# Optimization experiments

Measured on AMD Instinct MI355X. Metric: run time of the kernel, lower is better.

## Reference

```python
import jax, jax.numpy as jnp
import numpy as np

P2 = 8
BN_EPS = 1e-5


def _slice_maps(p2):
    # Faithfully reproduce the buggy fs[:, i*j-1] indexing: later loop
    # iterations overwrite earlier ones; slots never written stay zero.
    last = {}
    for i in range(1, p2 + 1):
        for j in range(1, p2 + 1):
            last[i * j - 1] = (i - 1, j - 1)
    src_i = np.zeros(p2 * p2, np.int32)
    src_j = np.zeros(p2 * p2, np.int32)
    mask = np.zeros(p2 * p2, np.float32)
    for k, (ii, jj) in last.items():
        src_i[k], src_j[k], mask[k] = ii, jj, 1.0
    # unslice: output patch (i,j) reads slot (i+1)*(j+1)-1
    uns = np.array([[(i + 1) * (j + 1) - 1 for j in range(p2)] for i in range(p2)], np.int32)
    return src_i, src_j, mask, uns


def setup_inputs() -> dict:
    key = jax.random.key(0)
    ks = jax.random.split(key, 16)
    C, N, p2 = 32, 8, P2
    s = 0.05
    inp = {
        "x": jax.random.normal(ks[0], (8, C, 512, 512), jnp.float32),
        "w30": jax.random.normal(ks[1], (N, C, 3, 3), jnp.float32) * s,
        "b30": jnp.zeros((N,), jnp.float32),
        "w10": jax.random.normal(ks[2], (C, C), jnp.float32) * s,
        "b10": jnp.zeros((C,), jnp.float32),
        "w11": jax.random.normal(ks[3], (N, N), jnp.float32) * s,
        "b11": jnp.zeros((N,), jnp.float32),
        "w12a": jax.random.normal(ks[4], (p2, p2 * p2), jnp.float32) * s,
        "b12a": jnp.zeros((p2,), jnp.float32),
        "w12b": jax.random.normal(ks[5], (p2, p2), jnp.float32) * s,
        "b12b": jnp.zeros((p2,), jnp.float32),
        "w12c": jax.random.normal(ks[6], (p2 * p2, p2), jnp.float32) * s,
        "b12c": jnp.zeros((p2 * p2,), jnp.float32),
        "w31": jax.random.normal(ks[7], (C, C), jnp.float32) * s,
        "b31": jnp.zeros((C,), jnp.float32),
        "bn_gamma": jnp.ones((C,), jnp.float32),
        "bn_beta": jnp.zeros((C,), jnp.float32),
        "bn_mean": jnp.zeros((C,), jnp.float32),
        "bn_var": jnp.ones((C,), jnp.float32),
    }
    return inp


def reference(x, w30, b30, w10, b10, w11, b11, w12a, b12a, w12b, b12b,
              w12c, b12c, w31, b31, bn_gamma, bn_beta, bn_mean, bn_var):
    p2 = P2
    b, C, H, W = x.shape
    h, wd = H // p2, W // p2
    L = h * wd
    N = w30.shape[0]
    src_i, src_j, mask_np, uns = _slice_maps(p2)

    # --- slice into patches (with the original's overwrite/zero semantics) ---
    patches = x.reshape(b, C, p2, h, p2, wd).transpose(0, 2, 4, 1, 3, 5)  # [b,p2,p2,C,h,w]
    fs = patches[:, src_i, src_j] * jnp.asarray(mask_np)[None, :, None, None, None]
    fs = fs.reshape(b * p2 * p2, C, h, wd)

    # --- graph_convolution ---
    B = jax.lax.conv_general_dilated(fs, w30, (1, 1), 'SAME',
            dimension_numbers=('NCHW', 'OIHW', 'NCHW')) + b30[None, :, None, None]
    B = jax.nn.relu(B)                                    # [bp, N, h, w]
    B1 = B.reshape(b * p2 * p2, N, L)
    fs1 = fs.reshape(b * p2 * p2, C, L)
    fs2 = jnp.einsum('bnl,bcl->bnc', B1, fs1)              # [bp, N, C]
    fs3 = jax.nn.relu(jnp.einsum('on,bnc->boc', w11, fs2) + b11[None, :, None])
    fs5 = jax.nn.relu(jnp.einsum('oc,bcn->bon', w10, fs3.transpose(0, 2, 1)) + b10[None, :, None])  # [bp,C,N]
    fs6 = jnp.einsum('bnl,bcn->bcl', B1, fs5)              # [bp, C, L]
    fs6 = fs6.reshape(b, p2 * p2, C, h, wd)

    fg = x.reshape(b, C, 8, H // 8, 8, W // 8).mean(axis=(3, 5))  # [b,C,8,8]
    fg1 = fg.reshape(b, C, p2 * p2).transpose(0, 2, 1)            # [b, p2^2, C]
    g = jax.nn.relu(jnp.einsum('ok,bkc->boc', w12a, fg1) + b12a[None, :, None])
    g = jax.nn.relu(jnp.einsum('ok,bkc->boc', w12b, g) + b12b[None, :, None])
    g = jax.nn.sigmoid(jnp.einsum('ok,bkc->boc', w12c, g) + b12c[None, :, None])  # [b,p2^2,C]
    out5 = g[:, :, :, None, None] * fs6                            # [b,p2^2,C,h,w]

    # --- unslice back to image (patch (i,j) reads slot (i+1)*(j+1)-1) ---
    gathered = out5[:, uns]                                        # [b,p2,p2,C,h,w]
    out = gathered.transpose(0, 3, 1, 4, 2, 5).reshape(b, C, H, W)

    # --- conv31: 1x1 conv + BatchNorm(eval) + ReLU, residual add ---
    y = jnp.einsum('oc,bchw->bohw', w31, out) + b31[None, :, None, None]
    y = (y - bn_mean[None, :, None, None]) * jax.lax.rsqrt(bn_var[None, :, None, None] + BN_EPS)
    y = jax.nn.relu(y * bn_gamma[None, :, None, None] + bn_beta[None, :, None, None])
    return y + x
```

## Files before the change

### kernel.cpp

```cpp
#include <hip/hip_runtime.h>
#include <math.h>
#include <stdint.h>

#define HW 512
#define NACT 30
#define NINACT 34

struct Maps {
    int src_i[64];
    int src_j[64];
    int mask[64];
    int aidx[64];
    int act_k[NACT];
    int inact_k[NINACT];
};

static Maps make_maps() {
    Maps m;
    for (int k = 0; k < 64; k++) { m.src_i[k]=0; m.src_j[k]=0; m.mask[k]=0; m.aidx[k]=-1; }
    for (int i = 1; i <= 8; i++)
        for (int j = 1; j <= 8; j++) {
            int k = i*j-1;
            m.src_i[k]=i-1; m.src_j[k]=j-1; m.mask[k]=1;
        }
    int cnt=0, icnt=0;
    for (int k=0;k<64;k++) {
        if (m.mask[k]) { m.aidx[k]=cnt; if (cnt < NACT) m.act_k[cnt]=k; cnt++; }
        else           { if (icnt < NINACT) m.inact_k[icnt]=k; icnt++; }
    }
    return m;
}

__global__ __launch_bounds__(256) void k_zero(float* __restrict__ p, int n) {
    int i = blockIdx.x*256 + threadIdx.x;
    if (i < n) p[i] = 0.f;
}

__global__ __launch_bounds__(256) void k_fg(const float* __restrict__ x, float* __restrict__ fgw, Maps m) {
    int blk = blockIdx.x;
    int q = blk % NINACT;
    int bc = blk / NINACT;
    int c = bc & 31;
    int b = bc >> 5;
    int k = m.inact_k[q];
    int pi = k >> 3, pj = k & 7;
    const float* xp = x + (size_t)(b*32+c)*HW*HW;
    int t = threadIdx.x;
    float s = 0.f;
    #pragma unroll
    for (int ii = 0; ii < 4; ii++) {
        int idx4 = t + 256*ii;
        int y = idx4 >> 4;
        int xx = (idx4 & 15) * 4;
        float4 v = *(const float4*)(xp + (size_t)(pi*64 + y)*HW + pj*64 + xx);
        s += v.x + v.y + v.z + v.w;
    }
    for (int off = 32; off > 0; off >>= 1) s += __shfl_down(s, off);
    __shared__ float p[4];
    if ((t & 63) == 0) p[t >> 6] = s;
    __syncthreads();
    if (t == 0) {
        float tot = p[0]+p[1]+p[2]+p[3];
        fgw[(b*64 + k)*32 + c] = tot * (1.0f/4096.0f);
    }
}

__global__ void k_g(const float* __restrict__ fgw,
                    const float* __restrict__ w12a, const float* __restrict__ b12a,
                    const float* __restrict__ w12b, const float* __restrict__ b12b,
                    const float* __restrict__ w12c, const float* __restrict__ b12c,
                    float* __restrict__ g) {
    int b = blockIdx.x;
    int c = threadIdx.x;
    if (c >= 32) return;
    float fg[64];
    #pragma unroll
    for (int k = 0; k < 64; k++) fg[k] = fgw[(b*64+k)*32 + c];
    float g1[8], g2[8];
    #pragma unroll
    for (int o = 0; o < 8; o++) {
        float v = b12a[o];
        #pragma unroll
        for (int k2 = 0; k2 < 64; k2++) v += w12a[o*64+k2]*fg[k2];
        g1[o] = fmaxf(v, 0.f);
    }
    #pragma unroll
    for (int o = 0; o < 8; o++) {
        float v = b12b[o];
        #pragma unroll
        for (int k2 = 0; k2 < 8; k2++) v += w12b[o*8+k2]*g1[k2];
        g2[o] = fmaxf(v, 0.f);
    }
    for (int o = 0; o < 64; o++) {
        float v = b12c[o];
        #pragma unroll
        for (int k2 = 0; k2 < 8; k2++) v += w12c[o*8+k2]*g2[k2];
        g[(b*64+o)*32 + c] = 1.f / (1.f + expf(-v));
    }
}

__global__ __launch_bounds__(256, 8) void k_conv(
        const float* __restrict__ x, const float* __restrict__ w30,
        const float* __restrict__ b30, float* __restrict__ B, Maps m) {
    int blk = blockIdx.x;
    int rt = blockIdx.y;
    int a = blk % NACT, b = blk / NACT;
    int k = m.act_k[a];
    int spi = m.src_i[k], spj = m.src_j[k];
    int r0 = rt*8;

    __shared__ float wlc[288];
    __shared__ __align__(16) float xs[4*10*72];

    int t = threadIdx.x;
    for (int idx = t; idx < 4*10*72; idx += 256) xs[idx] = 0.f;

    int col = t & 63, tl = t >> 6;
    float acc[2][8];
    #pragma unroll
    for (int rr=0; rr<2; rr++)
        #pragma unroll
        for (int n=0;n<8;n++) acc[rr][n]=0.f;

    const float* xb = x + (size_t)b*32*HW*HW;

    for (int c0 = 0; c0 < 32; c0 += 4) {
        __syncthreads();
        for (int idx = t; idx < 288; idx += 256) {
            int cc = idx / 72;
            int rem = idx - cc*72;
            wlc[idx] = w30[((rem & 7)*32 + c0 + cc)*9 + (rem >> 3)];
        }
        for (int idx = t; idx < 640; idx += 256) {
            int cc = idx / 160;
            int rem = idx - cc*160;
            int r = rem >> 4;
            int q = rem & 15;
            int pr = r0 - 1 + r;
            float4 v = make_float4(0.f,0.f,0.f,0.f);
            if (pr >= 0 && pr < 64)
                v = *(const float4*)(xb + (size_t)(c0+cc)*HW*HW + (size_t)(spi*64+pr)*HW + spj*64 + q*4);
            *(float4*)(xs + cc*720 + r*72 + 4 + q*4) = v;
        }
        __syncthreads();
        #pragma unroll
        for (int cc = 0; cc < 4; cc++) {
            const float* xrow = xs + cc*720 + (tl*2)*72 + 3 + col;
            const float* wb = wlc + cc*72;
            #pragma unroll
            for (int dy = 0; dy < 3; dy++) {
                float xa0 = xrow[dy*72 + 0];
                float xa1 = xrow[dy*72 + 1];
                float xa2 = xrow[dy*72 + 2];
                float xb0 = xrow[dy*72 + 72];
                float xb1 = xrow[dy*72 + 73];
                float xb2 = xrow[dy*72 + 74];
                #pragma unroll
                for (int dx = 0; dx < 3; dx++) {
                    float4 wa0 = *(const float4*)(wb + (dy*3+dx)*8);
                    float4 wa1 = *(const float4*)(wb + (dy*3+dx)*8 + 4);
                    float x0 = (dx==0) ? xa0 : ((dx==1) ? xa1 : xa2);
                    float x1 = (dx==0) ? xb0 : ((dx==1) ? xb1 : xb2);
                    acc[0][0] = fmaf(x0, wa0.x, acc[0][0]);
                    acc[0][1] = fmaf(x0, wa0.y, acc[0][1]);
                    acc[0][2] = fmaf(x0, wa0.z, acc[0][2]);
                    acc[0][3] = fmaf(x0, wa0.w, acc[0][3]);
                    acc[0][4] = fmaf(x0, wa1.x, acc[0][4]);
                    acc[0][5] = fmaf(x0, wa1.y, acc[0][5]);
                    acc[0][6] = fmaf(x0, wa1.z, acc[0][6]);
                    acc[0][7] = fmaf(x0, wa1.w, acc[0][7]);
                    acc[1][0] = fmaf(x1, wa0.x, acc[1][0]);
                    acc[1][1] = fmaf(x1, wa0.y, acc[1][1]);
                    acc[1][2] = fmaf(x1, wa0.z, acc[1][2]);
                    acc[1][3] = fmaf(x1, wa0.w, acc[1][3]);
                    acc[1][4] = fmaf(x1, wa1.x, acc[1][4]);
                    acc[1][5] = fmaf(x1, wa1.y, acc[1][5]);
                    acc[1][6] = fmaf(x1, wa1.z, acc[1][6]);
                    acc[1][7] = fmaf(x1, wa1.w, acc[1][7]);
                }
            }
        }
    }
    float* Bp = B + (size_t)(b*NACT+a)*8*4096;
    #pragma unroll
    for (int rr=0; rr<2; rr++) {
        int y = r0 + tl*2 + rr;
        #pragma unroll
        for (int n=0;n<8;n++)
            Bp[n*4096 + y*64 + col] = fmaxf(acc[rr][n] + b30[n], 0.f);
    }
}

__global__ __launch_bounds__(256, 8) void k_fs2a(
        const float* __restrict__ x, const float* __restrict__ B,
        float* __restrict__ fs2g, float* __restrict__ fgw, Maps m) {
    int blk = blockIdx.x;
    int rt = blockIdx.y;
    int a = blk % NACT, b = blk / NACT;
    int k = m.act_k[a];
    int spi = m.src_i[k], spj = m.src_j[k];
    int l0 = rt*128;

    __shared__ __align__(16) float xs[32*132];

    int t = threadIdx.x;
    const float* xb = x + (size_t)b*32*HW*HW;
    #pragma unroll
    for (int q4 = 0; q4 < 4; q4++) {
        int idx = t + 256*q4;
        int c = idx >> 5, lq = idx & 31;
        int l = l0 + lq*4;
        int y = l >> 6, xx = l & 63;
        float4 v = *(const float4*)(xb + (size_t)c*HW*HW + (size_t)(spi*64+y)*HW + spj*64 + xx);
        *(float4*)(xs + c*132 + lq*4) = v;
    }
    __syncthreads();

    int n = t >> 5, c = t & 31;
    const float4* Bg4 = (const float4*)(B + (size_t)(b*NACT+a)*8*4096 + (size_t)n*4096 + l0);
    const float4* xs4 = (const float4*)(xs + c*132);
    float facc = 0.f;
    #pragma unroll 4
    for (int q = 0; q < 32; q++) {
        float4 bv = Bg4[q];
        float4 xv = xs4[q];
        facc = fmaf(bv.x, xv.x, facc);
        facc = fmaf(bv.y, xv.y, facc);
        facc = fmaf(bv.z, xv.z, facc);
        facc = fmaf(bv.w, xv.w, facc);
    }
    atomicAdd(&fs2g[(size_t)(b*NACT+a)*256 + n*32 + c], facc);

    if (t < 32) {
        const float4* xc4 = (const float4*)(xs + t*132);
        float s = 0.f;
        #pragma unroll 4
        for (int q = 0; q < 32; q++) {
            float4 v = xc4[q];
            s += v.x + v.y + v.z + v.w;
        }
        atomicAdd(&fgw[(b*64 + k)*32 + t], s * (1.0f/4096.0f));
    }
}

__global__ __launch_bounds__(256) void k_fs3(
        const float* __restrict__ fs2g,
        const float* __restrict__ w11, const float* __restrict__ b11,
        const float* __restrict__ w10, const float* __restrict__ b10,
        float* __restrict__ fs5, Maps m) {
    int blk = blockIdx.x;
    int a = blk % NACT, b = blk / NACT;
    int k = m.act_k[a];
    __shared__ float fs2s[8*33], fs3s[8*33];
    int t = threadIdx.x;
    {
        int n = t >> 5, c = t & 31;
        fs2s[n*33+c] = fs2g[(size_t)(b*NACT+a)*256 + n*32 + c];
    }
    __syncthreads();
    {
        int o = t >> 5, c = t & 31;
        float v = b11[o];
        #pragma unroll
        for (int n=0;n<8;n++) v += w11[o*8+n]*fs2s[n*33+c];
        fs3s[o*33+c] = fmaxf(v, 0.f);
    }
    __syncthreads();
    {
        int cp = t >> 3, n = t & 7;
        float v = b10[cp];
        #pragma unroll
        for (int c=0;c<32;c++) v += w10[cp*32+c]*fs3s[n*33+c];
        fs5[((size_t)(b*64+k)*32 + cp)*8 + n] = fmaxf(v, 0.f);
    }
}

__global__ __launch_bounds__(256) void k_out(
        const float* __restrict__ x, const float* __restrict__ B,
        const float* __restrict__ fs5, const float* __restrict__ g,
        const float* __restrict__ w31, const float* __restrict__ b31,
        const float* __restrict__ gamma, const float* __restrict__ beta,
        const float* __restrict__ mean, const float* __restrict__ var,
        float* __restrict__ out, Maps m) {
    int blk = blockIdx.x;
    int rt = blockIdx.y;
    int h  = blockIdx.z;
    int ij = blk & 63, b = blk >> 6;
    int i = ij >> 3, j = ij & 7;
    int K = (i+1)*(j+1) - 1;
    int aK = m.aidx[K];
    __shared__ float Ms[128];
    __shared__ float ss2[16], sh2[16];
    int t = threadIdx.x;
    if (t < 128) {
        int ol = t >> 3, n = t & 7;
        int o = h*16 + ol;
        const float* f5 = fs5 + (size_t)(b*64+K)*32*8;
        const float* gg = g + (size_t)(b*64+K)*32;
        float v = 0.f;
        #pragma unroll
        for (int c=0;c<32;c++) v += w31[o*32+c]*gg[c]*f5[c*8+n];
        Ms[ol*8+n] = v;
    } else if (t < 144) {
        int ol = t - 128;
        int o = h*16 + ol;
        float sc = rsqrtf(var[o] + 1e-5f) * gamma[o];
        ss2[ol] = sc;
        sh2[ol] = (b31[o] - mean[o])*sc + beta[o];
    }
    __syncthreads();

    int hh = t >> 7;
    int gidx = t & 127;
    int r = gidx >> 4, q = gidx & 15;
    int y = rt*8 + r;
    int Y = i*64 + y;
    int X = j*64 + q*4;
    int obase = hh*8;
    const float* Bp = B + (size_t)(b*NACT+aK)*8*4096 + y*64 + q*4;
    const float* xb = x + ((size_t)(b*32 + h*16 + obase)*HW + Y)*HW + X;
    float* ob = out + ((size_t)(b*32 + h*16 + obase)*HW + Y)*HW + X;

    float4 Bv[8];
    #pragma unroll
    for (int n=0;n<8;n++) Bv[n] = *(const float4*)(Bp + n*4096);

    #pragma unroll 8
    for (int oo = 0; oo < 8; oo++) {
        int ol = obase + oo;
        float4 Ma = *(const float4*)(Ms + ol*8);
        float4 Mb = *(const float4*)(Ms + ol*8 + 4);
        float so = ss2[ol], ho = sh2[ol];
        float4 xv = *(const float4*)(xb + (size_t)oo*HW*HW);
        float4 yv;
        yv.x = Bv[0].x*Ma.x + Bv[1].x*Ma.y + Bv[2].x*Ma.z + Bv[3].x*Ma.w
             + Bv[4].x*Mb.x + Bv[5].x*Mb.y + Bv[6].x*Mb.z + Bv[7].x*Mb.w;
        yv.y = Bv[0].y*Ma.x + Bv[1].y*Ma.y + Bv[2].y*Ma.z + Bv[3].y*Ma.w
             + Bv[4].y*Mb.x + Bv[5].y*Mb.y + Bv[6].y*Mb.z + Bv[7].y*Mb.w;
        yv.z = Bv[0].z*Ma.x + Bv[1].z*Ma.y + Bv[2].z*Ma.z + Bv[3].z*Ma.w
             + Bv[4].z*Mb.x + Bv[5].z*Mb.y + Bv[6].z*Mb.z + Bv[7].z*Mb.w;
        yv.w = Bv[0].w*Ma.x + Bv[1].w*Ma.y + Bv[2].w*Ma.z + Bv[3].w*Ma.w
             + Bv[4].w*Mb.x + Bv[5].w*Mb.y + Bv[6].w*Mb.z + Bv[7].w*Mb.w;
        float4 res;
        res.x = fmaxf(yv.x*so + ho, 0.f) + xv.x;
        res.y = fmaxf(yv.y*so + ho, 0.f) + xv.y;
        res.z = fmaxf(yv.z*so + ho, 0.f) + xv.z;
        res.w = fmaxf(yv.w*so + ho, 0.f) + xv.w;
        *(float4*)(ob + (size_t)oo*HW*HW) = res;
    }
}

extern "C" void kernel_launch(void* const* d_in, const int* in_sizes, int n_in,
                              void* d_out, int out_size, void* d_ws, size_t ws_size,
                              hipStream_t stream) {
    const float* x    = (const float*)d_in[0];
    const float* w30  = (const float*)d_in[1];
    const float* b30  = (const float*)d_in[2];
    const float* w10  = (const float*)d_in[3];
    const float* b10  = (const float*)d_in[4];
    const float* w11  = (const float*)d_in[5];
    const float* b11  = (const float*)d_in[6];
    const float* w12a = (const float*)d_in[7];
    const float* b12a = (const float*)d_in[8];
    const float* w12b = (const float*)d_in[9];
    const float* b12b = (const float*)d_in[10];
    const float* w12c = (const float*)d_in[11];
    const float* b12c = (const float*)d_in[12];
    const float* w31  = (const float*)d_in[13];
    const float* b31  = (const float*)d_in[14];
    const float* gam  = (const float*)d_in[15];
    const float* bet  = (const float*)d_in[16];
    const float* mea  = (const float*)d_in[17];
    const float* var  = (const float*)d_in[18];
    float* out = (float*)d_out;

    float* ws   = (float*)d_ws;
    float* B    = ws;
    float* fs5  = B + 7864320;
    float* fgw  = fs5 + 131072;
    float* g    = fgw + 16384;
    float* fs2g = g + 16384;

    static Maps m = make_maps();

    k_zero<<<dim3(368),       256, 0, stream>>>(fgw, 94208);
    k_conv<<<dim3(240, 8),    256, 0, stream>>>(x, w30, b30, B, m);
    k_fs2a<<<dim3(240, 32),   256, 0, stream>>>(x, B, fs2g, fgw, m);
    k_fg  <<<dim3(8704),      256, 0, stream>>>(x, fgw, m);
    k_g   <<<dim3(8),          64, 0, stream>>>(fgw, w12a, b12a, w12b, b12b, w12c, b12c, g);
    k_fs3 <<<dim3(240),       256, 0, stream>>>(fs2g, w11, b11, w10, b10, fs5, m);
    k_out <<<dim3(512, 8, 2), 256, 0, stream>>>(x, B, fs5, g, w31, b31, gam, bet, mea, var, out, m);
}
```

Baseline: 629.8 us.

## Merge independent small kernels into fused multi-role launches

Combines the zeroing, 3x3 conv and inactive-patch pooling kernels into one launch whose block index picks the role. The fs3 and ADP-weight kernels are likewise merged into a single mid kernel. The zeroing now clears only the regions that are later accumulated into, fs2g and the active fgw slots. This cuts the launch count from seven to four and lets independent work share the GPU concurrently. In exchange, the merged kernel's shared-memory footprint and register limit now apply to the lighter roles as well.

```diff
diff --git a/kernel.cpp b/kernel.cpp
--- a/kernel.cpp
+++ b/kernel.cpp
@@ -5,6 +5,11 @@
 #define HW 512
 #define NACT 30
 #define NINACT 34
+
+#define CONV_BLOCKS 1920
+#define ZERO_BLOCKS 68
+#define FG_BLOCKS   8704
+#define KA_GRID (CONV_BLOCKS + ZERO_BLOCKS + FG_BLOCKS)
 
 struct Maps {
     int src_i[64];
@@ -31,163 +36,138 @@
     return m;
 }
 
-__global__ __launch_bounds__(256) void k_zero(float* __restrict__ p, int n) {
-    int i = blockIdx.x*256 + threadIdx.x;
-    if (i < n) p[i] = 0.f;
-}
-
-__global__ __launch_bounds__(256) void k_fg(const float* __restrict__ x, float* __restrict__ fgw, Maps m) {
-    int blk = blockIdx.x;
-    int q = blk % NINACT;
-    int bc = blk / NINACT;
-    int c = bc & 31;
-    int b = bc >> 5;
-    int k = m.inact_k[q];
-    int pi = k >> 3, pj = k & 7;
-    const float* xp = x + (size_t)(b*32+c)*HW*HW;
+__global__ __launch_bounds__(256, 8) void k_A(
+        const float* __restrict__ x, const float* __restrict__ w30,
+        const float* __restrict__ b30, float* __restrict__ B,
+        float* __restrict__ fgw, float* __restrict__ fs2g, Maps m) {
+    int gid = blockIdx.x;
     int t = threadIdx.x;
-    float s = 0.f;
-    #pragma unroll
-    for (int ii = 0; ii < 4; ii++) {
-        int idx4 = t + 256*ii;
-        int y = idx4 >> 4;
-        int xx = (idx4 & 15) * 4;
-        float4 v = *(const float4*)(xp + (size_t)(pi*64 + y)*HW + pj*64 + xx);
-        s += v.x + v.y + v.z + v.w;
-    }
-    for (int off = 32; off > 0; off >>= 1) s += __shfl_down(s, off);
-    __shared__ float p[4];
-    if ((t & 63) == 0) p[t >> 6] = s;
-    __syncthreads();
-    if (t == 0) {
-        float tot = p[0]+p[1]+p[2]+p[3];
-        fgw[(b*64 + k)*32 + c] = tot * (1.0f/4096.0f);
-    }
-}
-
-__global__ void k_g(const float* __restrict__ fgw,
-                    const float* __restrict__ w12a, const float* __restrict__ b12a,
-                    const float* __restrict__ w12b, const float* __restrict__ b12b,
-                    const float* __restrict__ w12c, const float* __restrict__ b12c,
-                    float* __restrict__ g) {
-    int b = blockIdx.x;
-    int c = threadIdx.x;
-    if (c >= 32) return;
-    float fg[64];
-    #pragma unroll
-    for (int k = 0; k < 64; k++) fg[k] = fgw[(b*64+k)*32 + c];
-    float g1[8], g2[8];
-    #pragma unroll
-    for (int o = 0; o < 8; o++) {
-        float v = b12a[o];
-        #pragma unroll
-        for (int k2 = 0; k2 < 64; k2++) v += w12a[o*64+k2]*fg[k2];
-        g1[o] = fmaxf(v, 0.f);
-    }
-    #pragma unroll
-    for (int o = 0; o < 8; o++) {
-        float v = b12b[o];
-        #pragma unroll
-        for (int k2 = 0; k2 < 8; k2++) v += w12b[o*8+k2]*g1[k2];
-        g2[o] = fmaxf(v, 0.f);
-    }
-    for (int o = 0; o < 64; o++) {
-        float v = b12c[o];
-        #pragma unroll
-        for (int k2 = 0; k2 < 8; k2++) v += w12c[o*8+k2]*g2[k2];
-        g[(b*64+o)*32 + c] = 1.f / (1.f + expf(-v));
-    }
-}
-
-__global__ __launch_bounds__(256, 8) void k_conv(
-        const float* __restrict__ x, const float* __restrict__ w30,
-        const float* __restrict__ b30, float* __restrict__ B, Maps m) {
-    int blk = blockIdx.x;
-    int rt = blockIdx.y;
-    int a = blk % NACT, b = blk / NACT;
-    int k = m.act_k[a];
-    int spi = m.src_i[k], spj = m.src_j[k];
-    int r0 = rt*8;
-
-    __shared__ float wlc[288];
-    __shared__ __align__(16) float xs[4*10*72];
-
-    int t = threadIdx.x;
-    for (int idx = t; idx < 4*10*72; idx += 256) xs[idx] = 0.f;
-
-    int col = t & 63, tl = t >> 6;
-    float acc[2][8];
-    #pragma unroll
-    for (int rr=0; rr<2; rr++)
-        #pragma unroll
-        for (int n=0;n<8;n++) acc[rr][n]=0.f;
-
-    const float* xb = x + (size_t)b*32*HW*HW;
-
-    for (int c0 = 0; c0 < 32; c0 += 4) {
-        __syncthreads();
-        for (int idx = t; idx < 288; idx += 256) {
-            int cc = idx / 72;
-            int rem = idx - cc*72;
-            wlc[idx] = w30[((rem & 7)*32 + c0 + cc)*9 + (rem >> 3)];
-        }
-        for (int idx = t; idx < 640; idx += 256) {
-            int cc = idx / 160;
-            int rem = idx - cc*160;
-            int r = rem >> 4;
-            int q = rem & 15;
-            int pr = r0 - 1 + r;
-            float4 v = make_float4(0.f,0.f,0.f,0.f);
-            if (pr >= 0 && pr < 64)
-                v = *(const float4*)(xb + (size_t)(c0+cc)*HW*HW + (size_t)(spi*64+pr)*HW + spj*64 + q*4);
-            *(float4*)(xs + cc*720 + r*72 + 4 + q*4) = v;
-        }
-        __syncthreads();
-        #pragma unroll
-        for (int cc = 0; cc < 4; cc++) {
-            const float* xrow = xs + cc*720 + (tl*2)*72 + 3 + col;
-            const float* wb = wlc + cc*72;
-            #pragma unroll
-            for (int dy = 0; dy < 3; dy++) {
-                float xa0 = xrow[dy*72 + 0];
-                float xa1 = xrow[dy*72 + 1];
-                float xa2 = xrow[dy*72 + 2];
-                float xb0 = xrow[dy*72 + 72];
-                float xb1 = xrow[dy*72 + 73];
-                float xb2 = xrow[dy*72 + 74];
+
+    if (gid < CONV_BLOCKS) {
+        int blk = gid >> 3;
+        int rt  = gid & 7;
+        int a = blk % NACT, b = blk / NACT;
+        int k = m.act_k[a];
+        int spi = m.src_i[k], spj = m.src_j[k];
+        int r0 = rt*8;
+
+        __shared__ float wlc[288];
+        __shared__ __align__(16) float xs[4*10*72];
+
+        for (int idx = t; idx < 4*10*72; idx += 256) xs[idx] = 0.f;
+
+        int col = t & 63, tl = t >> 6;
+        float acc[2][8];
+        #pragma unroll
+        for (int rr=0; rr<2; rr++)
+            #pragma unroll
+            for (int n=0;n<8;n++) acc[rr][n]=0.f;
+
+        const float* xb = x + (size_t)b*32*HW*HW;
+
+        for (int c0 = 0; c0 < 32; c0 += 4) {
+            __syncthreads();
+            for (int idx = t; idx < 288; idx += 256) {
+                int cc = idx / 72;
+                int rem = idx - cc*72;
+                wlc[idx] = w30[((rem & 7)*32 + c0 + cc)*9 + (rem >> 3)];
+            }
+            for (int idx = t; idx < 640; idx += 256) {
+                int cc = idx / 160;
+                int rem = idx - cc*160;
+                int r = rem >> 4;
+                int q = rem & 15;
+                int pr = r0 - 1 + r;
+                float4 v = make_float4(0.f,0.f,0.f,0.f);
+                if (pr >= 0 && pr < 64)
+                    v = *(const float4*)(xb + (size_t)(c0+cc)*HW*HW + (size_t)(spi*64+pr)*HW + spj*64 + q*4);
+                *(float4*)(xs + cc*720 + r*72 + 4 + q*4) = v;
+            }
+            __syncthreads();
+            #pragma unroll
+            for (int cc = 0; cc < 4; cc++) {
+                const float* xrow = xs + cc*720 + (tl*2)*72 + 3 + col;
+                const float* wb = wlc + cc*72;
                 #pragma unroll
-                for (int dx = 0; dx < 3; dx++) {
-                    float4 wa0 = *(const float4*)(wb + (dy*3+dx)*8);
-                    float4 wa1 = *(const float4*)(wb + (dy*3+dx)*8 + 4);
-                    float x0 = (dx==0) ? xa0 : ((dx==1) ? xa1 : xa2);
-                    float x1 = (dx==0) ? xb0 : ((dx==1) ? xb1 : xb2);
-                    acc[0][0] = fmaf(x0, wa0.x, acc[0][0]);
-                    acc[0][1] = fmaf(x0, wa0.y, acc[0][1]);
-                    acc[0][2] = fmaf(x0, wa0.z, acc[0][2]);
-                    acc[0][3] = fmaf(x0, wa0.w, acc[0][3]);
-                    acc[0][4] = fmaf(x0, wa1.x, acc[0][4]);
-                    acc[0][5] = fmaf(x0, wa1.y, acc[0][5]);
-                    acc[0][6] = fmaf(x0, wa1.z, acc[0][6]);
-                    acc[0][7] = fmaf(x0, wa1.w, acc[0][7]);
-                    acc[1][0] = fmaf(x1, wa0.x, acc[1][0]);
-                    acc[1][1] = fmaf(x1, wa0.y, acc[1][1]);
-                    acc[1][2] = fmaf(x1, wa0.z, acc[1][2]);
-                    acc[1][3] = fmaf(x1, wa0.w, acc[1][3]);
-                    acc[1][4] = fmaf(x1, wa1.x, acc[1][4]);
-                    acc[1][5] = fmaf(x1, wa1.y, acc[1][5]);
-                    acc[1][6] = fmaf(x1, wa1.z, acc[1][6]);
-                    acc[1][7] = fmaf(x1, wa1.w, acc[1][7]);
+                for (int dy = 0; dy < 3; dy++) {
+                    float xa0 = xrow[dy*72 + 0];
+                    float xa1 = xrow[dy*72 + 1];
+                    float xa2 = xrow[dy*72 + 2];
+                    float xb0 = xrow[dy*72 + 72];
+                    float xb1 = xrow[dy*72 + 73];
+                    float xb2 = xrow[dy*72 + 74];
+                    #pragma unroll
+                    for (int dx = 0; dx < 3; dx++) {
+                        float4 wa0 = *(const float4*)(wb + (dy*3+dx)*8);
+                        float4 wa1 = *(const float4*)(wb + (dy*3+dx)*8 + 4);
+                        float x0 = (dx==0) ? xa0 : ((dx==1) ? xa1 : xa2);
+                        float x1 = (dx==0) ? xb0 : ((dx==1) ? xb1 : xb2);
+                        acc[0][0] = fmaf(x0, wa0.x, acc[0][0]);
+                        acc[0][1] = fmaf(x0, wa0.y, acc[0][1]);
+                        acc[0][2] = fmaf(x0, wa0.z, acc[0][2]);
+                        acc[0][3] = fmaf(x0, wa0.w, acc[0][3]);
+                        acc[0][4] = fmaf(x0, wa1.x, acc[0][4]);
+                        acc[0][5] = fmaf(x0, wa1.y, acc[0][5]);
+                        acc[0][6] = fmaf(x0, wa1.z, acc[0][6]);
+                        acc[0][7] = fmaf(x0, wa1.w, acc[0][7]);
+                        acc[1][0] = fmaf(x1, wa0.x, acc[1][0]);
+                        acc[1][1] = fmaf(x1, wa0.y, acc[1][1]);
+                        acc[1][2] = fmaf(x1, wa0.z, acc[1][2]);
+                        acc[1][3] = fmaf(x1, wa0.w, acc[1][3]);
+                        acc[1][4] = fmaf(x1, wa1.x, acc[1][4]);
+                        acc[1][5] = fmaf(x1, wa1.y, acc[1][5]);
+                        acc[1][6] = fmaf(x1, wa1.z, acc[1][6]);
+                        acc[1][7] = fmaf(x1, wa1.w, acc[1][7]);
+                    }
                 }
             }
         }
-    }
-    float* Bp = B + (size_t)(b*NACT+a)*8*4096;
-    #pragma unroll
-    for (int rr=0; rr<2; rr++) {
-        int y = r0 + tl*2 + rr;
-        #pragma unroll
-        for (int n=0;n<8;n++)
-            Bp[n*4096 + y*64 + col] = fmaxf(acc[rr][n] + b30[n], 0.f);
+        float* Bp = B + (size_t)(b*NACT+a)*8*4096;
+        #pragma unroll
+        for (int rr=0; rr<2; rr++) {
+            int y = r0 + tl*2 + rr;
+            #pragma unroll
+            for (int n=0;n<8;n++)
+                Bp[n*4096 + y*64 + col] = fmaxf(acc[rr][n] + b30[n], 0.f);
+        }
+    } else if (gid < CONV_BLOCKS + ZERO_BLOCKS) {
+        int z = gid - CONV_BLOCKS;
+        if (z < 60) {
+            float4* p = (float4*)(fs2g + z*1024);
+            p[t] = make_float4(0.f,0.f,0.f,0.f);
+        } else {
+            int b = z - 60;
+            for (int idx = t; idx < 960; idx += 256) {
+                int a = idx >> 5, c = idx & 31;
+                fgw[(b*64 + m.act_k[a])*32 + c] = 0.f;
+            }
+        }
+    } else {
+        int id = gid - CONV_BLOCKS - ZERO_BLOCKS;
+        int q = id % NINACT;
+        int bc = id / NINACT;
+        int c = bc & 31;
+        int b = bc >> 5;
+        int k = m.inact_k[q];
+        int pi = k >> 3, pj = k & 7;
+        const float* xp = x + (size_t)(b*32+c)*HW*HW;
+        float s = 0.f;
+        #pragma unroll
+        for (int ii = 0; ii < 4; ii++) {
+            int idx4 = t + 256*ii;
+            int y = idx4 >> 4;
+            int xx = (idx4 & 15) * 4;
+            float4 v = *(const float4*)(xp + (size_t)(pi*64 + y)*HW + pj*64 + xx);
+            s += v.x + v.y + v.z + v.w;
+        }
+        for (int off = 32; off > 0; off >>= 1) s += __shfl_down(s, off);
+        __shared__ float p[4];
+        if ((t & 63) == 0) p[t >> 6] = s;
+        __syncthreads();
+        if (t == 0) {
+            float tot = p[0]+p[1]+p[2]+p[3];
+            fgw[(b*64 + k)*32 + c] = tot * (1.0f/4096.0f);
+        }
     }
 }
 
@@ -243,35 +223,70 @@
     }
 }
 
-__global__ __launch_bounds__(256) void k_fs3(
+__global__ __launch_bounds__(256) void k_mid(
         const float* __restrict__ fs2g,
         const float* __restrict__ w11, const float* __restrict__ b11,
         const float* __restrict__ w10, const float* __restrict__ b10,
-        float* __restrict__ fs5, Maps m) {
-    int blk = blockIdx.x;
-    int a = blk % NACT, b = blk / NACT;
-    int k = m.act_k[a];
-    __shared__ float fs2s[8*33], fs3s[8*33];
+        float* __restrict__ fs5,
+        const float* __restrict__ fgw,
+        const float* __restrict__ w12a, const float* __restrict__ b12a,
+        const float* __restrict__ w12b, const float* __restrict__ b12b,
+        const float* __restrict__ w12c, const float* __restrict__ b12c,
+        float* __restrict__ g, Maps m) {
+    int gid = blockIdx.x;
     int t = threadIdx.x;
-    {
-        int n = t >> 5, c = t & 31;
-        fs2s[n*33+c] = fs2g[(size_t)(b*NACT+a)*256 + n*32 + c];
-    }
-    __syncthreads();
-    {
-        int o = t >> 5, c = t & 31;
-        float v = b11[o];
-        #pragma unroll
-        for (int n=0;n<8;n++) v += w11[o*8+n]*fs2s[n*33+c];
-        fs3s[o*33+c] = fmaxf(v, 0.f);
-    }
-    __syncthreads();
-    {
-        int cp = t >> 3, n = t & 7;
-        float v = b10[cp];
-        #pragma unroll
-        for (int c=0;c<32;c++) v += w10[cp*32+c]*fs3s[n*33+c];
-        fs5[((size_t)(b*64+k)*32 + cp)*8 + n] = fmaxf(v, 0.f);
+    if (gid < 240) {
+        int a = gid % NACT, b = gid / NACT;
+        int k = m.act_k[a];
+        __shared__ float fs2s[8*33], fs3s[8*33];
+        {
+            int n = t >> 5, c = t & 31;
+            fs2s[n*33+c] = fs2g[(size_t)(b*NACT+a)*256 + n*32 + c];
+        }
+        __syncthreads();
+        {
+            int o = t >> 5, c = t & 31;
+            float v = b11[o];
+            #pragma unroll
+            for (int n=0;n<8;n++) v += w11[o*8+n]*fs2s[n*33+c];
+            fs3s[o*33+c] = fmaxf(v, 0.f);
+        }
+        __syncthreads();
+        {
+            int cp = t >> 3, n = t & 7;
+            float v = b10[cp];
+            #pragma unroll
+            for (int c=0;c<32;c++) v += w10[cp*32+c]*fs3s[n*33+c];
+            fs5[((size_t)(b*64+k)*32 + cp)*8 + n] = fmaxf(v, 0.f);
+        }
+    } else {
+        int b = gid - 240;
+        int c = t;
+        if (c >= 32) return;
+        float fg[64];
+        #pragma unroll
+        for (int k = 0; k < 64; k++) fg[k] = fgw[(b*64+k)*32 + c];
+        float g1[8], g2[8];
+        #pragma unroll
+        for (int o = 0; o < 8; o++) {
+            float v = b12a[o];
+            #pragma unroll
+            for (int k2 = 0; k2 < 64; k2++) v += w12a[o*64+k2]*fg[k2];
+            g1[o] = fmaxf(v, 0.f);
+        }
+        #pragma unroll
+        for (int o = 0; o < 8; o++) {
+            float v = b12b[o];
+            #pragma unroll
+            for (int k2 = 0; k2 < 8; k2++) v += w12b[o*8+k2]*g1[k2];
+            g2[o] = fmaxf(v, 0.f);
+        }
+        for (int o = 0; o < 64; o++) {
+            float v = b12c[o];
+            #pragma unroll
+            for (int k2 = 0; k2 < 8; k2++) v += w12c[o*8+k2]*g2[k2];
+            g[(b*64+o)*32 + c] = 1.f / (1.f + expf(-v));
+        }
     }
 }
 
@@ -383,11 +398,9 @@
 
     static Maps m = make_maps();
 
-    k_zero<<<dim3(368),       256, 0, stream>>>(fgw, 94208);
-    k_conv<<<dim3(240, 8),    256, 0, stream>>>(x, w30, b30, B, m);
+    k_A   <<<dim3(KA_GRID),   256, 0, stream>>>(x, w30, b30, B, fgw, fs2g, m);
     k_fs2a<<<dim3(240, 32),   256, 0, stream>>>(x, B, fs2g, fgw, m);
-    k_fg  <<<dim3(8704),      256, 0, stream>>>(x, fgw, m);
-    k_g   <<<dim3(8),          64, 0, stream>>>(fgw, w12a, b12a, w12b, b12b, w12c, b12c, g);
-    k_fs3 <<<dim3(240),       256, 0, stream>>>(fs2g, w11, b11, w10, b10, fs5, m);
+    k_mid <<<dim3(248),       256, 0, stream>>>(fs2g, w11, b11, w10, b10, fs5,
+                                                fgw, w12a, b12a, w12b, b12b, w12c, b12c, g, m);
     k_out <<<dim3(512, 8, 2), 256, 0, stream>>>(x, B, fs5, g, w31, b31, gam, bet, mea, var, out, m);
 }
```

Measured after the change: 615.4 us. 2.3% less time.
